# Kernel tuning notes

Hardware: AMD Instinct MI355X
Metric: run time of the kernel (lower is better)

## Reference

```python
import math
import jax, jax.numpy as jnp
import numpy as np

B, L, D, H, NL, V = 4, 1024, 1024, 16, 8, 32000
HD = D // H
EPS = 1e-5


def _sinusoidal_pe(length, dim):
    pos = jnp.arange(length, dtype=jnp.float32)[:, None]
    div = jnp.exp(jnp.arange(0, dim, 2, dtype=jnp.float32) * (-math.log(10000.0) / dim))
    pe = jnp.zeros((length, dim), dtype=jnp.float32)
    pe = pe.at[:, 0::2].set(jnp.sin(pos * div))
    pe = pe.at[:, 1::2].set(jnp.cos(pos * div))
    return pe


def _layer_norm(x, scale, bias):
    mu = jnp.mean(x, axis=-1, keepdims=True)
    var = jnp.mean(jnp.square(x - mu), axis=-1, keepdims=True)
    return (x - mu) * jax.lax.rsqrt(var + EPS) * scale + bias


def setup_inputs() -> dict:
    key = jax.random.key(0)
    ks = jax.random.split(key, 10)
    std = 0.02
    p = {
        "idx": jax.random.randint(ks[0], (B, L), 0, V),
        "emb": jax.random.normal(ks[1], (V, D), jnp.float32) * std,
        # per-layer stacked params (leading dim NL)
        "ln1_s": jnp.ones((NL, D), jnp.float32),
        "ln1_b": jnp.zeros((NL, D), jnp.float32),
        "wq": jax.random.normal(ks[2], (NL, D, D), jnp.float32) * std,
        "wk": jax.random.normal(ks[3], (NL, D, D), jnp.float32) * std,
        "wv": jax.random.normal(ks[4], (NL, D, D), jnp.float32) * std,
        "wo": jax.random.normal(ks[5], (NL, D, D), jnp.float32) * std,
        "ln2_s": jnp.ones((NL, D), jnp.float32),
        "ln2_b": jnp.zeros((NL, D), jnp.float32),
        "w1": jax.random.normal(ks[6], (NL, D, 4 * D), jnp.float32) * std,
        "b1": jnp.zeros((NL, 4 * D), jnp.float32),
        "w2": jax.random.normal(ks[7], (NL, 4 * D, D), jnp.float32) * std,
        "b2": jnp.zeros((NL, D), jnp.float32),
        "lnf_s": jnp.ones((D,), jnp.float32),
        "lnf_b": jnp.zeros((D,), jnp.float32),
        "head": jax.random.normal(ks[8], (D, V), jnp.float32) * std,
    }
    return p


def _forward(idx, emb, ln1_s, ln1_b, wq, wk, wv, wo, ln2_s, ln2_b, w1, b1, w2, b2, lnf_s, lnf_b, head):
    x = emb[idx] + _sinusoidal_pe(L, D)[None]  # [B,L,D]
    causal = jnp.tril(jnp.ones((L, L), dtype=bool))  # [L,L]
    neg_inf = jnp.float32(-jnp.inf)

    def block(x, p):
        (l1s, l1b, Wq, Wk, Wv, Wo, l2s, l2b, W1, B1, W2, B2) = p
        h = _layer_norm(x, l1s, l1b)
        q = (h @ Wq).reshape(B, L, H, HD)
        k = (h @ Wk).reshape(B, L, H, HD)
        v = (h @ Wv).reshape(B, L, H, HD)
        att = jnp.einsum("bihd,bjhd->bhij", q, k) / math.sqrt(HD)
        att = jnp.where(causal, att, neg_inf)
        att = jax.nn.softmax(att, axis=-1)
        y = jnp.einsum("bhij,bjhd->bihd", att, v).reshape(B, L, D)
        x = x + y @ Wo
        h = _layer_norm(x, l2s, l2b)
        x = x + jax.nn.gelu(h @ W1 + B1, approximate=False) @ W2 + B2
        return x, None

    params = (ln1_s, ln1_b, wq, wk, wv, wo, ln2_s, ln2_b, w1, b1, w2, b2)
    x, _ = jax.lax.scan(block, x, params)
    x = _layer_norm(x, lnf_s, lnf_b)
    return x @ head  # [B,L,V]


def reference(idx, emb, ln1_s, ln1_b, wq, wk, wv, wo, ln2_s, ln2_b, w1, b1, w2, b2, lnf_s, lnf_b, head):
    return _forward(idx, emb, ln1_s, ln1_b, wq, wk, wv, wo, ln2_s, ln2_b, w1, b1, w2, b2, lnf_s, lnf_b, head)
```

## Files before the change

### kernel.cpp

```cpp
#include <hip/hip_runtime.h>
#include <hip/hip_bf16.h>
#include <math.h>

typedef __bf16 bf16_t;
typedef __attribute__((ext_vector_type(8))) __bf16 bf16x8;
typedef __attribute__((ext_vector_type(4))) __bf16 bf16x4;
typedef __attribute__((ext_vector_type(4))) float f32x4;

#define B_  4
#define L_  1024
#define D_  1024
#define H_  16
#define HD_ 64
#define NL_ 8
#define V_  32000
#define FF_ 4096

__global__ __launch_bounds__(256) void embed_kernel(const int* __restrict__ idx,
                                                    const float* __restrict__ emb,
                                                    float* __restrict__ x) {
  int token = blockIdx.x;
  int l = token & (L_ - 1);
  int id = idx[token];
  const float* erow = emb + (size_t)id * D_;
  float* xrow = x + (size_t)token * D_;
  int d0 = threadIdx.x * 4;
#pragma unroll
  for (int j = 0; j < 4; ++j) {
    int d = d0 + j;
    int i = d >> 1;
    float freq = expf((float)(2 * i) * (-9.210340371976184f / (float)D_));
    float ang = (float)l * freq;
    float pe = (d & 1) ? cosf(ang) : sinf(ang);
    xrow[d] = erow[d] + pe;
  }
}

__global__ __launch_bounds__(256) void ln_kernel(const float* __restrict__ x,
                                                 const float* __restrict__ gamma,
                                                 const float* __restrict__ beta,
                                                 bf16_t* __restrict__ out) {
  int row = blockIdx.x;
  int t = threadIdx.x;
  float4 v = ((const float4*)(x + (size_t)row * D_))[t];
  float va[4] = {v.x, v.y, v.z, v.w};
  float s = va[0] + va[1] + va[2] + va[3];
  float ss = va[0]*va[0] + va[1]*va[1] + va[2]*va[2] + va[3]*va[3];
#pragma unroll
  for (int m = 1; m < 64; m <<= 1) {
    s  += __shfl_xor(s, m);
    ss += __shfl_xor(ss, m);
  }
  __shared__ float red[8];
  int wid = t >> 6, lane = t & 63;
  if (lane == 0) { red[wid] = s; red[4 + wid] = ss; }
  __syncthreads();
  s  = red[0] + red[1] + red[2] + red[3];
  ss = red[4] + red[5] + red[6] + red[7];
  float mu  = s * (1.0f / D_);
  float var = fmaxf(ss * (1.0f / D_) - mu * mu, 0.0f);
  float rstd = rsqrtf(var + 1e-5f);
  int d0 = t * 4;
  bf16_t* orow = out + (size_t)row * D_ + d0;
#pragma unroll
  for (int j = 0; j < 4; ++j) {
    int d = d0 + j;
    orow[j] = (bf16_t)((va[j] - mu) * rstd * gamma[d] + beta[d]);
  }
}

__device__ __forceinline__ void tr64_body(const float* __restrict__ in, bf16_t* __restrict__ out,
                                          int K, int ldin, int n0, int k0) {
  __shared__ bf16_t tile[64][66];
  int tx = threadIdx.x, ty = threadIdx.y;
#pragma unroll
  for (int r = 0; r < 4; ++r) {
    int kk = ty + r * 16;
    float4 v = *(const float4*)(in + (size_t)(k0 + kk) * ldin + n0 + tx * 4);
    tile[kk][tx * 4 + 0] = (bf16_t)v.x;
    tile[kk][tx * 4 + 1] = (bf16_t)v.y;
    tile[kk][tx * 4 + 2] = (bf16_t)v.z;
    tile[kk][tx * 4 + 3] = (bf16_t)v.w;
  }
  __syncthreads();
#pragma unroll
  for (int r = 0; r < 4; ++r) {
    int nn = ty + r * 16;
    bf16x4 w;
    w[0] = tile[tx * 4 + 0][nn];
    w[1] = tile[tx * 4 + 1][nn];
    w[2] = tile[tx * 4 + 2][nn];
    w[3] = tile[tx * 4 + 3][nn];
    *(bf16x4*)(out + (size_t)(n0 + nn) * K + k0 + tx * 4) = w;
  }
}

__global__ void transpose64_k(const float* __restrict__ in, size_t base,
                              bf16_t* __restrict__ out, int K, int ldin) {
  tr64_body(in + base, out, K, ldin, blockIdx.x * 64, blockIdx.y * 64);
}

__global__ void transpose_all(const float* __restrict__ wq, const float* __restrict__ wk,
                              const float* __restrict__ wv, const float* __restrict__ wo,
                              const float* __restrict__ w1, const float* __restrict__ w2,
                              int lbase, bf16_t* __restrict__ outbase, size_t lstride) {
  int b = blockIdx.x;
  int li = b / 3072, t = b % 3072;
  int l = lbase + li;
  bf16_t* wl = outbase + (size_t)li * lstride;
  const size_t wofD = (size_t)l * D_ * D_;
  const size_t wofF = (size_t)l * D_ * FF_;
  const float* in; bf16_t* out; int K, ldin, x, y;
  if (t < 768) {
    int z = t >> 8, tt = t & 255;
    in = (z == 0 ? wq : z == 1 ? wk : wv) + wofD;
    out = wl + (size_t)z * D_ * D_;
    K = D_; ldin = D_; x = tt & 15; y = tt >> 4;
  } else if (t < 1024) {
    int tt = t - 768;
    in = wo + wofD; out = wl + 3145728;
    K = D_; ldin = D_; x = tt & 15; y = tt >> 4;
  } else if (t < 2048) {
    int tt = t - 1024;
    in = w1 + wofF; out = wl + 4194304;
    K = D_; ldin = FF_; x = tt & 63; y = tt >> 6;
  } else {
    int tt = t - 2048;
    in = w2 + wofF; out = wl + 8388608;
    K = FF_; ldin = D_; x = tt & 15; y = tt >> 4;
  }
  tr64_body(in, out, K, ldin, x * 64, y * 64);
}

__device__ __forceinline__ void gload_lds16(const bf16_t* g, bf16_t* lds) {
  __builtin_amdgcn_global_load_lds(
      (const __attribute__((address_space(1))) void*)g,
      (__attribute__((address_space(3))) void*)(void*)lds,
      16, 0, 0);
}

__device__ __forceinline__ void remap_block(int& bn, int& bm) {
  const int gx = gridDim.x, gy = gridDim.y;
  int lin = blockIdx.y * gx + blockIdx.x;
  int nwg = gx * gy;
  int q8 = nwg >> 3, r8 = nwg & 7;
  int xcd = lin & 7, pos = lin >> 3;
  int wg = (xcd < r8 ? xcd * (q8 + 1) : r8 * (q8 + 1) + (xcd - r8) * q8) + pos;
  if ((gy & 7) == 0) {
    int per = gx << 3;
    int grp = wg / per, win = wg % per;
    bm = (grp << 3) + (win & 7);
    bn = win >> 3;
  } else { bn = wg % gx; bm = wg / gx; }
}

template <int EPI>
__global__ __launch_bounds__(256) void gemm_bt_kernel(
    const bf16_t* __restrict__ A, const bf16_t* __restrict__ Bt,
    bf16_t* __restrict__ outb, float* __restrict__ outf,
    const float* __restrict__ bias, int M, int Nst, int K, int col0) {
  int bn, bm; remap_block(bn, bm);
  const int kz = blockIdx.z, KS = gridDim.z;
  const int Kc = K / KS;
  const int kbeg = kz * Kc, kend = kbeg + Kc;
  const int tid = threadIdx.x, wid = tid >> 6, lane = tid & 63;
  const int wm = wid >> 1, wn = wid & 1;
  const int l15 = lane & 15, l4 = lane >> 4;

  __shared__ __align__(16) bf16_t As[128 * 32];
  __shared__ __align__(16) bf16_t Bs[128 * 32];

  f32x4 acc[4][4] = {};

  const bf16_t* Ablk = A  + (size_t)(bm * 128) * K;
  const bf16_t* Bblk = Bt + (size_t)(bn * 128) * K;
  const int srow = lane >> 2;
  const int skof = (lane & 3) * 8;

  for (int k0 = kbeg; k0 < kend; k0 += 32) {
#pragma unroll
    for (int c = 0; c < 2; ++c) {
      int chunk = wid * 2 + c;
      int row = chunk * 16 + srow;
      gload_lds16(Ablk + (size_t)row * K + k0 + skof, As + chunk * 512);
      gload_lds16(Bblk + (size_t)row * K + k0 + skof, Bs + chunk * 512);
    }
    __syncthreads();

    bf16x8 af[4], bfv[4];
#pragma unroll
    for (int i = 0; i < 4; ++i)
      af[i] = *(const bf16x8*)(As + (wm * 64 + i * 16 + l15) * 32 + l4 * 8);
#pragma unroll
    for (int j = 0; j < 4; ++j)
      bfv[j] = *(const bf16x8*)(Bs + (wn * 64 + j * 16 + l15) * 32 + l4 * 8);
#pragma unroll
    for (int i = 0; i < 4; ++i)
#pragma unroll
      for (int j = 0; j < 4; ++j)
        acc[i][j] = __builtin_amdgcn_mfma_f32_16x16x32_bf16(af[i], bfv[j], acc[i][j], 0, 0, 0);
    __syncthreads();
  }

  const int row_base = bm * 128 + wm * 64;
  const int col_base = col0 + bn * 128 + wn * 64 + l15;
#pragma unroll
  for (int i = 0; i < 4; ++i) {
#pragma unroll
    for (int j = 0; j < 4; ++j) {
      int col = col_base + j * 16;
#pragma unroll
      for (int r = 0; r < 4; ++r) {
        int row = row_base + i * 16 + l4 * 4 + r;
        float val = acc[i][j][r];
        if (EPI == 3 && kz == 0) val += bias[col];
        atomicAdd(&outf[(size_t)row * Nst + col], val);
      }
    }
  }
}

template <int EPI>
__global__ __launch_bounds__(512, 2) void gemm256_kernel(
    const bf16_t* __restrict__ A, const bf16_t* __restrict__ Bt,
    bf16_t* __restrict__ outb, float* __restrict__ outf,
    const float* __restrict__ bias, int M, int Nst, int K, int col0) {
  int bn, bm; remap_block(bn, bm);
  const int tid = threadIdx.x, wid = tid >> 6, lane = tid & 63;
  const int wm = wid >> 2, wn = wid & 3;
  const int l15 = lane & 15, l4 = lane >> 4;

  __shared__ __align__(16) bf16_t smem[65536];

  f32x4 acc[8][4] = {};

  const bf16_t* Ab = A  + (size_t)(bm * 256) * K;
  const bf16_t* Bb = Bt + (size_t)(bn * 256) * K;
  const int NT = K >> 6;

  const int srow = tid >> 3;
  const int sx8  = tid & 7;
  const int xrd  = l15 & 7;

  auto stage_rows = [&](int t, int mat, int R) {
    const bf16_t* g = mat ? Bb : Ab;
    bf16_t* l = smem + (t & 1) * 32768 + mat * 16384 + R * 64;
    int row = R + srow;
    int gs  = sx8 ^ (row & 7);
    gload_lds16(g + (size_t)row * K + t * 64 + gs * 8, l + wid * 512);
  };
  auto stA_SP0 = [&](int t) { stage_rows(t, 0, 0);   stage_rows(t, 0, 128); };
  auto stA_SP1 = [&](int t) { stage_rows(t, 0, 64);  stage_rows(t, 0, 192); };
  auto stB_H0  = [&](int t) { stage_rows(t, 1, 0);   stage_rows(t, 1, 64);  };
  auto stB_H1  = [&](int t) { stage_rows(t, 1, 128); stage_rows(t, 1, 192); };

  stA_SP0(0); stB_H0(0); stA_SP1(0); stB_H1(0);
  stA_SP0(1); stB_H0(1); stA_SP1(1);
  asm volatile("s_waitcnt vmcnt(6)" ::: "memory");
  __builtin_amdgcn_s_barrier();

  bf16x8 af[4][2], bfr[4][2];

  auto rdB = [&](const bf16_t* sB, int nh) {
#pragma unroll
    for (int n = 0; n < 2; ++n)
#pragma unroll
      for (int ks = 0; ks < 2; ++ks)
        bfr[nh * 2 + n][ks] = *(const bf16x8*)(sB + (wn * 64 + (nh * 2 + n) * 16 + l15) * 64
                                                  + ((ks * 4 + l4) ^ xrd) * 8);
  };
  auto rdA = [&](const bf16_t* sA, int mh) {
#pragma unroll
    for (int m = 0; m < 4; ++m)
#pragma unroll
      for (int ks = 0; ks < 2; ++ks)
        af[m][ks] = *(const bf16x8*)(sA + (wm * 128 + mh * 64 + m * 16 + l15) * 64
                                        + ((ks * 4 + l4) ^ xrd) * 8);
  };
  auto mma = [&](int mh, int nh) {
    asm volatile("s_waitcnt lgkmcnt(0)" ::: "memory");
    __builtin_amdgcn_sched_barrier(0);
    __builtin_amdgcn_s_setprio(1);
#pragma unroll
    for (int m = 0; m < 4; ++m)
#pragma unroll
      for (int n = 0; n < 2; ++n)
#pragma unroll
        for (int ks = 0; ks < 2; ++ks)
          acc[mh * 4 + m][nh * 2 + n] = __builtin_amdgcn_mfma_f32_16x16x32_bf16(
              af[m][ks], bfr[nh * 2 + n][ks], acc[mh * 4 + m][nh * 2 + n], 0, 0, 0);
    __builtin_amdgcn_s_setprio(0);
  };

  const int NI = NT >> 1;
  for (int it = 0; it < NI; ++it) {
    const int T0 = 2 * it, T1 = 2 * it + 1;
    const bool pre = (it + 1 < NI);
    const bf16_t* sA0 = smem;
    const bf16_t* sB0 = smem + 16384;
    const bf16_t* sA1 = smem + 32768;
    const bf16_t* sB1 = smem + 49152;

    rdB(sB0, 0); rdA(sA0, 0);
    stB_H1(T1);
    __builtin_amdgcn_s_barrier();
    mma(0, 0);
    __builtin_amdgcn_s_barrier();
    rdB(sB0, 1);
    if (pre) stA_SP0(T0 + 2);
    __builtin_amdgcn_s_barrier();
    mma(0, 1);
    __builtin_amdgcn_s_barrier();
    rdA(sA0, 1);
    if (pre) stB_H0(T0 + 2);
    __builtin_amdgcn_s_barrier();
    mma(1, 0);
    __builtin_amdgcn_s_barrier();
    if (pre) stA_SP1(T0 + 2);
    __builtin_amdgcn_s_barrier();
    mma(1, 1);
    if (pre) { asm volatile("s_waitcnt vmcnt(6)" ::: "memory"); }
    else     { asm volatile("s_waitcnt vmcnt(0)" ::: "memory"); }
    __builtin_amdgcn_s_barrier();

    rdB(sB1, 0); rdA(sA1, 0);
    if (pre) stB_H1(T0 + 2);
    __builtin_amdgcn_s_barrier();
    mma(0, 0);
    __builtin_amdgcn_s_barrier();
    rdB(sB1, 1);
    if (pre) stA_SP0(T1 + 2);
    __builtin_amdgcn_s_barrier();
    mma(0, 1);
    __builtin_amdgcn_s_barrier();
    rdA(sA1, 1);
    if (pre) stB_H0(T1 + 2);
    __builtin_amdgcn_s_barrier();
    mma(1, 0);
    __builtin_amdgcn_s_barrier();
    if (pre) stA_SP1(T1 + 2);
    __builtin_amdgcn_s_barrier();
    mma(1, 1);
    if (pre) { asm volatile("s_waitcnt vmcnt(6)" ::: "memory"); }
    __builtin_amdgcn_s_barrier();
  }

  const int row_base = bm * 256 + wm * 128;
#pragma unroll
  for (int m = 0; m < 8; ++m) {
#pragma unroll
    for (int n = 0; n < 4; ++n) {
      int colg = bn * 256 + wn * 64 + n * 16 + l15;
#pragma unroll
      for (int r = 0; r < 4; ++r) {
        int row = row_base + m * 16 + l4 * 4 + r;
        float val = acc[m][n][r];
        if (EPI == 4) {
          outf[(size_t)row * Nst + col0 + colg] = val;
        } else if (EPI == 2) {
          int col = col0 + colg;
          float v2 = val + bias[col];
          v2 = 0.5f * v2 * (1.0f + erff(v2 * 0.7071067811865475f));
          outb[(size_t)row * Nst + col] = (bf16_t)v2;
        } else {
          int buf = colg >> 10;
          int lc  = colg & 1023;
          (outb + (size_t)buf * 4194304)[(size_t)row * 1024 + lc] = (bf16_t)val;
        }
      }
    }
  }
}

__global__ __launch_bounds__(512) void attn_kernel(
    const bf16_t* __restrict__ q, const bf16_t* __restrict__ k,
    const bf16_t* __restrict__ v, bf16_t* __restrict__ y) {
  int bid = blockIdx.x;
  int qt = bid & 7;
  int h  = (bid >> 3) & (H_ - 1);
  int b  = bid >> 7;
  int tid = threadIdx.x, wid = tid >> 6, lane = tid & 63;
  int l15 = lane & 15, l4 = lane >> 4;

  __shared__ __align__(16) bf16_t Ks[64 * 72];
  __shared__ __align__(16) bf16_t Vs[64 * 72];
  __shared__ __align__(16) bf16_t Ps[8][16 * 72];

  const int qrow0 = qt * 128 + wid * 16;
  const int qmax  = qrow0 + 15;
  const size_t bh = ((size_t)b * L_ * H_ + h) * HD_;

  bf16x8 qf[2];
#pragma unroll
  for (int c = 0; c < 2; ++c)
    qf[c] = *(const bf16x8*)(q + bh + (size_t)(qrow0 + l15) * (H_ * HD_) + c * 32 + l4 * 8);

  float m_r[4] = {-INFINITY, -INFINITY, -INFINITY, -INFINITY};
  float l_r[4] = {0.f, 0.f, 0.f, 0.f};
  f32x4 oacc[4] = {};

  const int ktmax = 2 * qt + 1;
  for (int kt = 0; kt <= ktmax; ++kt) {
    __syncthreads();
    int kbase = kt * 64;
    {
      int j = tid >> 3;
      int dof = (tid & 7) * 8;
      const size_t src = bh + (size_t)(kbase + j) * (H_ * HD_) + dof;
      *(bf16x8*)(Ks + j * 72 + dof) = *(const bf16x8*)(k + src);
      bf16x8 vv = *(const bf16x8*)(v + src);
      int colb = (j + dof) & 63;
#pragma unroll
      for (int jj = 0; jj < 8; ++jj) Vs[(dof + jj) * 72 + colb] = vv[jj];
    }
    __syncthreads();

    if (kbase > qmax) continue;

    f32x4 sacc[4] = {};
#pragma unroll
    for (int c = 0; c < 2; ++c) {
#pragma unroll
      for (int t = 0; t < 4; ++t) {
        bf16x8 kf = *(const bf16x8*)(Ks + (t * 16 + l15) * 72 + c * 32 + l4 * 8);
        sacc[t] = __builtin_amdgcn_mfma_f32_16x16x32_bf16(qf[c], kf, sacc[t], 0, 0, 0);
      }
    }

    float tmax[4] = {-INFINITY, -INFINITY, -INFINITY, -INFINITY};
#pragma unroll
    for (int t = 0; t < 4; ++t) {
#pragma unroll
      for (int r = 0; r < 4; ++r) {
        float sv = sacc[t][r] * 0.125f;
        int kj = kbase + t * 16 + l15;
        int qi = qrow0 + l4 * 4 + r;
        if (kj > qi) sv = -INFINITY;
        sacc[t][r] = sv;
        tmax[r] = fmaxf(tmax[r], sv);
      }
    }
#pragma unroll
    for (int r = 0; r < 4; ++r) {
#pragma unroll
      for (int md = 1; md < 16; md <<= 1)
        tmax[r] = fmaxf(tmax[r], __shfl_xor(tmax[r], md));
    }
    float alpha[4], tsum[4];
#pragma unroll
    for (int r = 0; r < 4; ++r) {
      float mn = fmaxf(m_r[r], tmax[r]);
      alpha[r] = expf(m_r[r] - mn);
      m_r[r] = mn;
      tsum[r] = 0.f;
    }
#pragma unroll
    for (int t = 0; t < 4; ++t) {
#pragma unroll
      for (int r = 0; r < 4; ++r) {
        float p = expf(sacc[t][r] - m_r[r]);
        tsum[r] += p;
        Ps[wid][(l4 * 4 + r) * 72 + t * 16 + l15] = (bf16_t)p;
      }
    }
#pragma unroll
    for (int r = 0; r < 4; ++r) {
#pragma unroll
      for (int md = 1; md < 16; md <<= 1)
        tsum[r] += __shfl_xor(tsum[r], md);
      l_r[r] = l_r[r] * alpha[r] + tsum[r];
    }
#pragma unroll
    for (int t = 0; t < 4; ++t)
#pragma unroll
      for (int r = 0; r < 4; ++r)
        oacc[t][r] *= alpha[r];

#pragma unroll
    for (int c = 0; c < 2; ++c) {
      bf16x8 pf = *(const bf16x8*)(&Ps[wid][l15 * 72 + c * 32 + l4 * 8]);
#pragma unroll
      for (int t = 0; t < 4; ++t) {
        int d = t * 16 + l15;
        int jb = c * 32 + l4 * 8;
        bf16x8 vf = *(const bf16x8*)(Vs + d * 72 + ((jb + (d & 56)) & 63));
        oacc[t] = __builtin_amdgcn_mfma_f32_16x16x32_bf16(pf, vf, oacc[t], 0, 0, 0);
      }
    }
  }

#pragma unroll
  for (int t = 0; t < 4; ++t) {
#pragma unroll
    for (int r = 0; r < 4; ++r) {
      int row = qrow0 + l4 * 4 + r;
      int d = t * 16 + l15;
      y[bh + (size_t)row * (H_ * HD_) + d] = (bf16_t)(oacc[t][r] / l_r[r]);
    }
  }
}

extern "C" void kernel_launch(void* const* d_in, const int* in_sizes, int n_in,
                              void* d_out, int out_size, void* d_ws, size_t ws_size,
                              hipStream_t stream) {
  (void)in_sizes; (void)n_in; (void)out_size;
  const int*   idx   = (const int*)d_in[0];
  const float* emb   = (const float*)d_in[1];
  const float* ln1_s = (const float*)d_in[2];
  const float* ln1_b = (const float*)d_in[3];
  const float* wq    = (const float*)d_in[4];
  const float* wk    = (const float*)d_in[5];
  const float* wv    = (const float*)d_in[6];
  const float* wo    = (const float*)d_in[7];
  const float* ln2_s = (const float*)d_in[8];
  const float* ln2_b = (const float*)d_in[9];
  const float* w1    = (const float*)d_in[10];
  const float* b1    = (const float*)d_in[11];
  const float* w2    = (const float*)d_in[12];
  const float* b2    = (const float*)d_in[13];
  const float* lnf_s = (const float*)d_in[14];
  const float* lnf_b = (const float*)d_in[15];
  const float* headw = (const float*)d_in[16];
  float* out = (float*)d_out;

  char* ws = (char*)d_ws;
  const size_t XO  = 0;
  const size_t HBO = XO  + 16777216;
  const size_t QBO = HBO + 8388608;
  const size_t KBO = QBO + 8388608;
  const size_t VBO = KBO + 8388608;
  const size_t YBO = VBO + 8388608;
  const size_t GBO = QBO;
  const size_t WTO = YBO + 8388608;
  const size_t LBYTES = 25165824;
  const size_t LELEMS = LBYTES / 2;
  const bool prepass = ws_size >= WTO + (size_t)NL_ * LBYTES;

  float*  X   = (float*)(ws + XO);
  bf16_t* Hb  = (bf16_t*)(ws + HBO);
  bf16_t* Qb  = (bf16_t*)(ws + QBO);
  bf16_t* Kb  = (bf16_t*)(ws + KBO);
  bf16_t* Vb  = (bf16_t*)(ws + VBO);
  bf16_t* Yb  = (bf16_t*)(ws + YBO);
  bf16_t* Gb  = (bf16_t*)(ws + GBO);
  bf16_t* Wbase = (bf16_t*)(ws + WTO);
  bf16_t* WT    = (bf16_t*)(ws + WTO);

  const int M = B_ * L_;
  const dim3 tb16(16, 16);

  embed_kernel<<<M, 256, 0, stream>>>(idx, emb, X);

  if (prepass)
    transpose_all<<<NL_ * 3072, tb16, 0, stream>>>(wq, wk, wv, wo, w1, w2, 0, Wbase, LELEMS);

  for (int l = 0; l < NL_; ++l) {
    bf16_t* wl = prepass ? (Wbase + (size_t)l * LELEMS) : Wbase;
    bf16_t* qkvT = wl;
    bf16_t* woT  = wl + 3145728;
    bf16_t* w1T  = wl + 4194304;
    bf16_t* w2T  = wl + 8388608;

    ln_kernel<<<M, 256, 0, stream>>>(X, ln1_s + (size_t)l * D_, ln1_b + (size_t)l * D_, Hb);

    if (!prepass)
      transpose_all<<<3072, tb16, 0, stream>>>(wq, wk, wv, wo, w1, w2, l, Wbase, 0);

    gemm256_kernel<5><<<dim3(3*D_/256, M/256), 512, 0, stream>>>(Hb, qkvT, Qb, nullptr, nullptr, M, D_, D_, 0);

    attn_kernel<<<B_ * H_ * (L_/128), 512, 0, stream>>>(Qb, Kb, Vb, Yb);

    gemm_bt_kernel<1><<<dim3(D_/128, M/128, 2), 256, 0, stream>>>(Yb, woT, nullptr, X, nullptr, M, D_, D_, 0);

    ln_kernel<<<M, 256, 0, stream>>>(X, ln2_s + (size_t)l * D_, ln2_b + (size_t)l * D_, Hb);

    gemm256_kernel<2><<<dim3(FF_/256, M/256), 512, 0, stream>>>(Hb, w1T, Gb, nullptr, b1 + (size_t)l * FF_, M, FF_, D_, 0);

    gemm_bt_kernel<3><<<dim3(D_/128, M/128, 4), 256, 0, stream>>>(Gb, w2T, nullptr, X, b2 + (size_t)l * D_, M, D_, FF_, 0);
  }

  ln_kernel<<<M, 256, 0, stream>>>(X, lnf_s, lnf_b, Hb);

  size_t avail = (ws_size > WTO) ? (ws_size - WTO) : 0;
  long long maxcols = (long long)(avail / ((size_t)D_ * 2));
  int chunk = (int)((maxcols / 256) * 256);
  if (chunk > V_) chunk = V_;
  if (chunk < 256) chunk = 256;
  for (int n0 = 0; n0 < V_; n0 += chunk) {
    int nc = (V_ - n0 < chunk) ? (V_ - n0) : chunk;
    transpose64_k<<<dim3(nc/64, D_/64), tb16, 0, stream>>>(headw, (size_t)n0, WT, D_, V_);
    gemm256_kernel<4><<<dim3(nc/256, M/256), 512, 0, stream>>>(Hb, WT, nullptr, out, nullptr, M, V_, D_, n0);
  }
}
```

Before: 2.953 ms.

## Replace split-K atomics with partial buffers reduced inside fused residual+layernorm

The split-K out-projection and FFN2 GEMMs now write per-split partial sums to separate fp32 buffers instead of issuing atomicAdds into the residual. A new ln_red_kernel sums those partials plus bias into X and applies the following layernorm in the same pass. Separately, attention softmax switches to exp2f with a log2e-folded scale, the gemm256 pipeline gains an explicit lgkmcnt wait before a barrier, and the head transpose is done in one pass when the workspace is large enough. In exchange it needs a much larger workspace and adds extra fp32 partial-buffer traffic.

New measurement: 2.649 ms. -10.3%, faster.

```diff
diff --git a/kernel.cpp b/kernel.cpp
--- a/kernel.cpp
+++ b/kernel.cpp
@@ -62,6 +62,52 @@
   float rstd = rsqrtf(var + 1e-5f);
   int d0 = t * 4;
   bf16_t* orow = out + (size_t)row * D_ + d0;
+#pragma unroll
+  for (int j = 0; j < 4; ++j) {
+    int d = d0 + j;
+    orow[j] = (bf16_t)((va[j] - mu) * rstd * gamma[d] + beta[d]);
+  }
+}
+
+template <int NP>
+__global__ __launch_bounds__(256) void ln_red_kernel(
+    float* __restrict__ x, const float* __restrict__ part,
+    const float* __restrict__ bias,
+    const float* __restrict__ gamma, const float* __restrict__ beta,
+    bf16_t* __restrict__ out) {
+  int row = blockIdx.x;
+  int t = threadIdx.x;
+  size_t rb = (size_t)row * D_;
+  float4 v = ((const float4*)(x + rb))[t];
+  float va[4] = {v.x, v.y, v.z, v.w};
+#pragma unroll
+  for (int p = 0; p < NP; ++p) {
+    float4 pv = ((const float4*)(part + (size_t)p * 4194304 + rb))[t];
+    va[0] += pv.x; va[1] += pv.y; va[2] += pv.z; va[3] += pv.w;
+  }
+  if (bias) {
+    float4 bv = ((const float4*)bias)[t];
+    va[0] += bv.x; va[1] += bv.y; va[2] += bv.z; va[3] += bv.w;
+  }
+  ((float4*)(x + rb))[t] = make_float4(va[0], va[1], va[2], va[3]);
+  float s = va[0] + va[1] + va[2] + va[3];
+  float ss = va[0]*va[0] + va[1]*va[1] + va[2]*va[2] + va[3]*va[3];
+#pragma unroll
+  for (int m = 1; m < 64; m <<= 1) {
+    s  += __shfl_xor(s, m);
+    ss += __shfl_xor(ss, m);
+  }
+  __shared__ float red[8];
+  int wid = t >> 6, lane = t & 63;
+  if (lane == 0) { red[wid] = s; red[4 + wid] = ss; }
+  __syncthreads();
+  s  = red[0] + red[1] + red[2] + red[3];
+  ss = red[4] + red[5] + red[6] + red[7];
+  float mu  = s * (1.0f / D_);
+  float var = fmaxf(ss * (1.0f / D_) - mu * mu, 0.0f);
+  float rstd = rsqrtf(var + 1e-5f);
+  int d0 = t * 4;
+  bf16_t* orow = out + rb + d0;
 #pragma unroll
   for (int j = 0; j < 4; ++j) {
     int d = d0 + j;
@@ -213,8 +259,12 @@
       for (int r = 0; r < 4; ++r) {
         int row = row_base + i * 16 + l4 * 4 + r;
         float val = acc[i][j][r];
-        if (EPI == 3 && kz == 0) val += bias[col];
-        atomicAdd(&outf[(size_t)row * Nst + col], val);
+        if (EPI == 5) {
+          outf[(size_t)kz * 4194304 + (size_t)row * Nst + col] = val;
+        } else {
+          if (EPI == 3 && kz == 0) val += bias[col];
+          atomicAdd(&outf[(size_t)row * Nst + col], val);
+        }
       }
     }
   }
@@ -303,6 +353,7 @@
 
     rdB(sB0, 0); rdA(sA0, 0);
     stB_H1(T1);
+    asm volatile("s_waitcnt lgkmcnt(8)" ::: "memory");
     __builtin_amdgcn_s_barrier();
     mma(0, 0);
     __builtin_amdgcn_s_barrier();
@@ -325,6 +376,7 @@
 
     rdB(sB1, 0); rdA(sA1, 0);
     if (pre) stB_H1(T0 + 2);
+    asm volatile("s_waitcnt lgkmcnt(8)" ::: "memory");
     __builtin_amdgcn_s_barrier();
     mma(0, 0);
     __builtin_amdgcn_s_barrier();
@@ -389,6 +441,7 @@
   const int qrow0 = qt * 128 + wid * 16;
   const int qmax  = qrow0 + 15;
   const size_t bh = ((size_t)b * L_ * H_ + h) * HD_;
+  const float SCL = 0.125f * 1.44269504f;
 
   bf16x8 qf[2];
 #pragma unroll
@@ -432,7 +485,7 @@
     for (int t = 0; t < 4; ++t) {
 #pragma unroll
       for (int r = 0; r < 4; ++r) {
-        float sv = sacc[t][r] * 0.125f;
+        float sv = sacc[t][r] * SCL;
         int kj = kbase + t * 16 + l15;
         int qi = qrow0 + l4 * 4 + r;
         if (kj > qi) sv = -INFINITY;
@@ -450,7 +503,7 @@
 #pragma unroll
     for (int r = 0; r < 4; ++r) {
       float mn = fmaxf(m_r[r], tmax[r]);
-      alpha[r] = expf(m_r[r] - mn);
+      alpha[r] = exp2f(m_r[r] - mn);
       m_r[r] = mn;
       tsum[r] = 0.f;
     }
@@ -458,7 +511,7 @@
     for (int t = 0; t < 4; ++t) {
 #pragma unroll
       for (int r = 0; r < 4; ++r) {
-        float p = expf(sacc[t][r] - m_r[r]);
+        float p = exp2f(sacc[t][r] - m_r[r]);
         tsum[r] += p;
         Ps[wid][(l4 * 4 + r) * 72 + t * 16 + l15] = (bf16_t)p;
       }
@@ -534,7 +587,13 @@
   const size_t WTO = YBO + 8388608;
   const size_t LBYTES = 25165824;
   const size_t LELEMS = LBYTES / 2;
-  const bool prepass = ws_size >= WTO + (size_t)NL_ * LBYTES;
+  const size_t PREB = (size_t)NL_ * LBYTES;
+  const size_t WOPO = WTO + PREB;
+  const size_t F2PO = WOPO + 33554432;
+  const size_t HWTO = F2PO + 67108864;
+  const size_t NEED = HWTO + (size_t)V_ * D_ * 2;
+  const bool big = ws_size >= NEED;
+  const bool prepass = big || (ws_size >= WTO + PREB);
 
   float*  X   = (float*)(ws + XO);
   bf16_t* Hb  = (bf16_t*)(ws + HBO);
@@ -544,7 +603,8 @@
   bf16_t* Yb  = (bf16_t*)(ws + YBO);
   bf16_t* Gb  = (bf16_t*)(ws + GBO);
   bf16_t* Wbase = (bf16_t*)(ws + WTO);
-  bf16_t* WT    = (bf16_t*)(ws + WTO);
+  float*  woP = (float*)(ws + WOPO);
+  float*  f2P = (float*)(ws + F2PO);
 
   const int M = B_ * L_;
   const dim3 tb16(16, 16);
@@ -561,7 +621,12 @@
     bf16_t* w1T  = wl + 4194304;
     bf16_t* w2T  = wl + 8388608;
 
-    ln_kernel<<<M, 256, 0, stream>>>(X, ln1_s + (size_t)l * D_, ln1_b + (size_t)l * D_, Hb);
+    if (big && l > 0) {
+      ln_red_kernel<4><<<M, 256, 0, stream>>>(X, f2P, b2 + (size_t)(l - 1) * D_,
+                                              ln1_s + (size_t)l * D_, ln1_b + (size_t)l * D_, Hb);
+    } else {
+      ln_kernel<<<M, 256, 0, stream>>>(X, ln1_s + (size_t)l * D_, ln1_b + (size_t)l * D_, Hb);
+    }
 
     if (!prepass)
       transpose_all<<<3072, tb16, 0, stream>>>(wq, wk, wv, wo, w1, w2, l, Wbase, 0);
@@ -570,25 +635,41 @@
 
     attn_kernel<<<B_ * H_ * (L_/128), 512, 0, stream>>>(Qb, Kb, Vb, Yb);
 
-    gemm_bt_kernel<1><<<dim3(D_/128, M/128, 2), 256, 0, stream>>>(Yb, woT, nullptr, X, nullptr, M, D_, D_, 0);
-
-    ln_kernel<<<M, 256, 0, stream>>>(X, ln2_s + (size_t)l * D_, ln2_b + (size_t)l * D_, Hb);
+    if (big) {
+      gemm_bt_kernel<5><<<dim3(D_/128, M/128, 2), 256, 0, stream>>>(Yb, woT, nullptr, woP, nullptr, M, D_, D_, 0);
+      ln_red_kernel<2><<<M, 256, 0, stream>>>(X, woP, nullptr,
+                                              ln2_s + (size_t)l * D_, ln2_b + (size_t)l * D_, Hb);
+    } else {
+      gemm_bt_kernel<1><<<dim3(D_/128, M/128, 2), 256, 0, stream>>>(Yb, woT, nullptr, X, nullptr, M, D_, D_, 0);
+      ln_kernel<<<M, 256, 0, stream>>>(X, ln2_s + (size_t)l * D_, ln2_b + (size_t)l * D_, Hb);
+    }
 
     gemm256_kernel<2><<<dim3(FF_/256, M/256), 512, 0, stream>>>(Hb, w1T, Gb, nullptr, b1 + (size_t)l * FF_, M, FF_, D_, 0);
 
-    gemm_bt_kernel<3><<<dim3(D_/128, M/128, 4), 256, 0, stream>>>(Gb, w2T, nullptr, X, b2 + (size_t)l * D_, M, D_, FF_, 0);
-  }
-
-  ln_kernel<<<M, 256, 0, stream>>>(X, lnf_s, lnf_b, Hb);
-
-  size_t avail = (ws_size > WTO) ? (ws_size - WTO) : 0;
-  long long maxcols = (long long)(avail / ((size_t)D_ * 2));
-  int chunk = (int)((maxcols / 256) * 256);
-  if (chunk > V_) chunk = V_;
-  if (chunk < 256) chunk = 256;
-  for (int n0 = 0; n0 < V_; n0 += chunk) {
-    int nc = (V_ - n0 < chunk) ? (V_ - n0) : chunk;
-    transpose64_k<<<dim3(nc/64, D_/64), tb16, 0, stream>>>(headw, (size_t)n0, WT, D_, V_);
-    gemm256_kernel<4><<<dim3(nc/256, M/256), 512, 0, stream>>>(Hb, WT, nullptr, out, nullptr, M, V_, D_, n0);
-  }
-}
+    if (big) {
+      gemm_bt_kernel<5><<<dim3(D_/128, M/128, 4), 256, 0, stream>>>(Gb, w2T, nullptr, f2P, nullptr, M, D_, FF_, 0);
+    } else {
+      gemm_bt_kernel<3><<<dim3(D_/128, M/128, 4), 256, 0, stream>>>(Gb, w2T, nullptr, X, b2 + (size_t)l * D_, M, D_, FF_, 0);
+    }
+  }
+
+  if (big) {
+    ln_red_kernel<4><<<M, 256, 0, stream>>>(X, f2P, b2 + (size_t)(NL_ - 1) * D_, lnf_s, lnf_b, Hb);
+    bf16_t* HWT = (bf16_t*)(ws + HWTO);
+    transpose64_k<<<dim3(V_/64, D_/64), tb16, 0, stream>>>(headw, 0, HWT, D_, V_);
+    gemm256_kernel<4><<<dim3(V_/256, M/256), 512, 0, stream>>>(Hb, HWT, nullptr, out, nullptr, M, V_, D_, 0);
+  } else {
+    ln_kernel<<<M, 256, 0, stream>>>(X, lnf_s, lnf_b, Hb);
+    bf16_t* WT = (bf16_t*)(ws + WTO);
+    size_t avail = (ws_size > WTO) ? (ws_size - WTO) : 0;
+    long long maxcols = (long long)(avail / ((size_t)D_ * 2));
+    int chunk = (int)((maxcols / 256) * 256);
+    if (chunk > V_) chunk = V_;
+    if (chunk < 256) chunk = 256;
+    for (int n0 = 0; n0 < V_; n0 += chunk) {
+      int nc = (V_ - n0 < chunk) ? (V_ - n0) : chunk;
+      transpose64_k<<<dim3(nc/64, D_/64), tb16, 0, stream>>>(headw, (size_t)n0, WT, D_, V_);
+      gemm256_kernel<4><<<dim3(nc/256, M/256), 512, 0, stream>>>(Hb, WT, nullptr, out, nullptr, M, V_, D_, n0);
+    }
+  }
+}
```
